# Performance work log

Measured on AMD Instinct MI355X. Metric: run time of the kernel, lower is better.

Reference implementation:

```python
import jax, jax.numpy as jnp
import numpy as np

VOCAB = 128
HID = 1024
STD = 0.01


def setup_inputs() -> dict:
    key = jax.random.key(0)
    ks = jax.random.split(key, 9)
    X = jax.random.randint(ks[0], (64, 512), 0, VOCAB, dtype=jnp.int32)
    def w(k, shape):
        return jax.random.normal(k, shape, dtype=jnp.float32) * STD
    return {
        "X": X,
        # reset gate
        "Wr_x": w(ks[1], (VOCAB, HID)), "Wr_h": w(ks[2], (HID, HID)), "b_r": jnp.zeros(HID, jnp.float32),
        # update gate
        "Wz_x": w(ks[3], (VOCAB, HID)), "Wz_h": w(ks[4], (HID, HID)), "b_z": jnp.zeros(HID, jnp.float32),
        # candidate
        "Wh_x": w(ks[5], (VOCAB, HID)), "Wh_h": w(ks[6], (HID, HID)), "b_h": jnp.zeros(HID, jnp.float32),
        # output head
        "W_o": w(ks[7], (HID, VOCAB)), "b_o": jnp.zeros(VOCAB, jnp.float32),
    }


def reference(X, Wr_x, Wr_h, b_r, Wz_x, Wz_h, b_z, Wh_x, Wh_h, b_h, W_o, b_o):
    B, T = X.shape
    # one-hot encode all timesteps: (T, B, V)
    Xoh = jax.nn.one_hot(X.T, VOCAB, dtype=jnp.float32)

    def step(h, x_t):
        # x_t: (B, V), h: (B, H)
        r = jax.nn.sigmoid(x_t @ Wr_x + h @ Wr_h + b_r)
        z = jax.nn.sigmoid(x_t @ Wz_x + h @ Wz_h + b_z)
        h_tilde = jnp.tanh(x_t @ Wh_x + (r * h) @ Wh_h + b_h)
        h_new = z * h + (1.0 - z) * h_tilde
        out = h_new @ W_o + b_o  # (B, V)
        return h_new, out

    h0 = jnp.zeros((B, HID), jnp.float32)
    _, outs = jax.lax.scan(step, h0, Xoh)  # outs: (T, B, V)
    return jnp.transpose(outs, (1, 0, 2))  # (B, T, V)
```

## Files before the change

### kernel.cpp

```cpp
#include <hip/hip_runtime.h>

#define HID   1024
#define TLEN  512
#define VOC   128
#define NRZ   32
#define NH    32
#define NO    8
#define NBLK  (NRZ + NH + NO)
#define LDSK  1032
#define HBUF  (64 * HID)
#define NHB   8

typedef __bf16 bf16_t;
typedef __attribute__((ext_vector_type(8))) __bf16 bf16x8;
typedef __attribute__((ext_vector_type(4))) float  f32x4;

__device__ __forceinline__ float sigmoid_fast(float x) {
  return 1.0f / (1.0f + __expf(-x));
}
__device__ __forceinline__ float tanh_fast(float x) {
  float e = __expf(-2.0f * x);
  return (1.0f - e) / (1.0f + e);
}

union PairU { bf16_t b[2]; unsigned u; };
union ZPair { float f[2]; unsigned long long u; };


__device__ __forceinline__ void wait_fence(const unsigned* flags, int n, unsigned tgt) {
  if ((threadIdx.x >> 6) == 0) {
    const int lane = threadIdx.x & 63;
    for (;;) {
      unsigned g = tgt;
      if (lane < n)
        g = __hip_atomic_load(&flags[lane], __ATOMIC_RELAXED, __HIP_MEMORY_SCOPE_AGENT);
      if (__all(g >= tgt)) break;
      __builtin_amdgcn_s_sleep(1);
    }
    __builtin_amdgcn_fence(__ATOMIC_ACQUIRE, "agent");
  }
  __syncthreads();
}

__device__ __forceinline__ void wait_nofence(const unsigned* flags, int n, unsigned tgt) {
  if ((threadIdx.x >> 6) == 0) {
    const int lane = threadIdx.x & 63;
    for (;;) {
      unsigned g = tgt;
      if (lane < n)
        g = __hip_atomic_load(&flags[lane], __ATOMIC_RELAXED, __HIP_MEMORY_SCOPE_AGENT);
      if (__all(g >= tgt)) break;
      __builtin_amdgcn_s_sleep(1);
    }
  }
  __syncthreads();
}

__device__ __forceinline__ void wait_rh_out(const unsigned* rfl, const unsigned* ofl,
                                            unsigned tgt, unsigned otgt) {
  if ((threadIdx.x >> 6) == 0) {
    const int lane = threadIdx.x & 63;
    for (;;) {
      bool ok = true;
      if (lane < 32)
        ok = __hip_atomic_load(&rfl[lane], __ATOMIC_RELAXED, __HIP_MEMORY_SCOPE_AGENT) >= tgt;
      else if (lane < 40)
        ok = __hip_atomic_load(&ofl[lane - 32], __ATOMIC_RELAXED, __HIP_MEMORY_SCOPE_AGENT) >= otgt;
      if (__all(ok)) break;
      __builtin_amdgcn_s_sleep(1);
    }
    __builtin_amdgcn_fence(__ATOMIC_ACQUIRE, "agent");
  }
  __syncthreads();
}

__device__ __forceinline__ void publish_rel(unsigned* f, unsigned v) {
  __syncthreads();
  if (threadIdx.x == 0)
    __hip_atomic_store(f, v, __ATOMIC_RELEASE, __HIP_MEMORY_SCOPE_AGENT);
}
__device__ __forceinline__ void publish_rlx(unsigned* f, unsigned v) {
  __syncthreads();
  if (threadIdx.x == 0)
    __hip_atomic_store(f, v, __ATOMIC_RELAXED, __HIP_MEMORY_SCOPE_AGENT);
}

#define MFMA(a, b, c) __builtin_amdgcn_mfma_f32_16x16x32_bf16((a), (b), (c), 0, 0, 0)

__global__ void __launch_bounds__(256)
gru_rz(const int* __restrict__ X,
       const float* __restrict__ Wr_x, const float* __restrict__ Wr_h, const float* __restrict__ b_r,
       const float* __restrict__ Wz_x, const float* __restrict__ Wz_h, const float* __restrict__ b_z,
       const float* __restrict__ Wh_x, const float* __restrict__ Wh_h, const float* __restrict__ b_h,
       const float* __restrict__ W_o,  const float* __restrict__ b_o,
       float* __restrict__ out,
       bf16_t* __restrict__ h0, bf16_t* __restrict__ rh_bf, float* __restrict__ z_f32,
       unsigned* __restrict__ flags)
{
  __shared__ __align__(16) bf16_t Wbuf[2 * 32 * LDSK];

  unsigned* hfl = flags;
  unsigned* rfl = flags + 32;
  unsigned* zfl = flags + 64;
  unsigned* ofl = flags + 96;

  const int blk  = blockIdx.x;
  const int tid  = threadIdx.x;
  const int lane = tid & 63;
  const int wv   = tid >> 6;
  const int n16  = lane & 15;
  const int q    = lane >> 4;

  const int aoff = (wv * 16 + n16) * HID + q * 8;

  int bi[4];
#pragma unroll
  for (int i = 0; i < 4; ++i) bi[i] = wv * 16 + q * 4 + i;

  if (blk < NRZ) {
    const int c0 = blk * 32;
    for (int idx = tid; idx < 32 * HID; idx += 256) {
      int n = idx & 31, k = idx >> 5;
      int r = (n & 1) * 16 + (n >> 1);
      Wbuf[r * LDSK + k]               = (bf16_t)Wr_h[k * HID + c0 + n];
      Wbuf[32 * LDSK + r * LDSK + k]   = (bf16_t)Wz_h[k * HID + c0 + n];
    }
    __syncthreads();

    const int j0 = c0 + 2 * n16;
    const float br0 = b_r[j0], br1 = b_r[j0 + 1];
    const float bz0 = b_z[j0], bz1 = b_z[j0 + 1];
    const bf16_t* wr0 = &Wbuf[n16 * LDSK + q * 8];
    const bf16_t* wr1 = &Wbuf[(16 + n16) * LDSK + q * 8];
    const bf16_t* wz0 = &Wbuf[32 * LDSK + n16 * LDSK + q * 8];
    const bf16_t* wz1 = &Wbuf[32 * LDSK + (16 + n16) * LDSK + q * 8];

    for (int t = 0; t < TLEN; ++t) {
      float gr0[4], gr1[4], gz0[4], gz1[4];
#pragma unroll
      for (int i = 0; i < 4; ++i) {
        int xb = X[bi[i] * TLEN + t];
        gr0[i] = Wr_x[xb * HID + j0];
        gr1[i] = Wr_x[xb * HID + j0 + 1];
        gz0[i] = Wz_x[xb * HID + j0];
        gz1[i] = Wz_x[xb * HID + j0 + 1];
      }
      wait_fence(hfl, NH, (unsigned)t);
      const bf16_t* hslot = h0 + (t & (NHB - 1)) * HBUF;
      const bf16_t* hrow  = hslot + aoff;
      bf16x8 areg[32];
#pragma unroll
      for (int kk = 0; kk < 32; ++kk)
        areg[kk] = *reinterpret_cast<const bf16x8*>(hrow + kk * 32);
      f32x4 a0 = {0.f,0.f,0.f,0.f}, a1 = {0.f,0.f,0.f,0.f};
#pragma unroll
      for (int kk = 0; kk < 32; ++kk) {
        bf16x8 w0 = *reinterpret_cast<const bf16x8*>(wr0 + kk * 32);
        bf16x8 w1 = *reinterpret_cast<const bf16x8*>(wr1 + kk * 32);
        a0 = MFMA(areg[kk], w0, a0);
        a1 = MFMA(areg[kk], w1, a1);
      }
#pragma unroll
      for (int i = 0; i < 4; ++i) {
        int b = bi[i];
        float r0 = sigmoid_fast(a0[i] + br0 + gr0[i]);
        float r1 = sigmoid_fast(a1[i] + br1 + gr1[i]);
        PairU hp = *reinterpret_cast<const PairU*>(hslot + b * HID + j0);
        PairU c;
        c.b[0] = (bf16_t)(r0 * (float)hp.b[0]);
        c.b[1] = (bf16_t)(r1 * (float)hp.b[1]);
        *reinterpret_cast<PairU*>(rh_bf + b * HID + j0) = c;
      }
      publish_rel(&rfl[blk], (unsigned)(t + 1));

      f32x4 c0v = {0.f,0.f,0.f,0.f}, c1v = {0.f,0.f,0.f,0.f};
#pragma unroll
      for (int kk = 0; kk < 32; ++kk) {
        bf16x8 w0 = *reinterpret_cast<const bf16x8*>(wz0 + kk * 32);
        bf16x8 w1 = *reinterpret_cast<const bf16x8*>(wz1 + kk * 32);
        c0v = MFMA(areg[kk], w0, c0v);
        c1v = MFMA(areg[kk], w1, c1v);
      }
#pragma unroll
      for (int i = 0; i < 4; ++i) {
        ZPair zp;
        zp.f[0] = sigmoid_fast(c0v[i] + bz0 + gz0[i]);
        zp.f[1] = sigmoid_fast(c1v[i] + bz1 + gz1[i]);
        __hip_atomic_store((unsigned long long*)(z_f32 + bi[i] * HID + j0), zp.u,
                           __ATOMIC_RELAXED, __HIP_MEMORY_SCOPE_AGENT);
      }
      publish_rlx(&zfl[blk], (unsigned)(t + 1));
    }
  } else if (blk < NRZ + NH) {
    const int hb = blk - NRZ;
    const int c0 = hb * 32;
    for (int idx = tid; idx < 32 * HID; idx += 256) {
      int n = idx & 31, k = idx >> 5;
      int r = (n & 1) * 16 + (n >> 1);
      Wbuf[r * LDSK + k] = (bf16_t)Wh_h[k * HID + c0 + n];
    }
    __syncthreads();

    const int j0 = c0 + 2 * n16;
    const float bh0 = b_h[j0], bh1 = b_h[j0 + 1];
    const bf16_t* wh0 = &Wbuf[n16 * LDSK + q * 8];
    const bf16_t* wh1 = &Wbuf[(16 + n16) * LDSK + q * 8];
    const bf16_t* rhrow = rh_bf + aoff;

    f32x4 hm0 = {0.f,0.f,0.f,0.f}, hm1 = {0.f,0.f,0.f,0.f};

    for (int t = 0; t < TLEN; ++t) {
      float gh0[4], gh1[4];
#pragma unroll
      for (int i = 0; i < 4; ++i) {
        int xb = X[bi[i] * TLEN + t];
        gh0[i] = Wh_x[xb * HID + j0];
        gh1[i] = Wh_x[xb * HID + j0 + 1];
      }
      unsigned otgt = (t + 1 >= NHB) ? (unsigned)(t + 2 - NHB) : 0u;
      wait_rh_out(rfl, ofl, (unsigned)(t + 1), otgt);
      bf16x8 areg[32];
#pragma unroll
      for (int kk = 0; kk < 32; ++kk)
        areg[kk] = *reinterpret_cast<const bf16x8*>(rhrow + kk * 32);
      f32x4 ah0 = {0.f,0.f,0.f,0.f}, ah1 = {0.f,0.f,0.f,0.f};
#pragma unroll
      for (int kk = 0; kk < 32; ++kk) {
        bf16x8 w0 = *reinterpret_cast<const bf16x8*>(wh0 + kk * 32);
        bf16x8 w1 = *reinterpret_cast<const bf16x8*>(wh1 + kk * 32);
        ah0 = MFMA(areg[kk], w0, ah0);
        ah1 = MFMA(areg[kk], w1, ah1);
      }
      wait_nofence(zfl, NRZ, (unsigned)(t + 1));
      bf16_t* hnext = h0 + ((t + 1) & (NHB - 1)) * HBUF;
#pragma unroll
      for (int i = 0; i < 4; ++i) {
        ZPair zp;
        zp.u = __hip_atomic_load((const unsigned long long*)(z_f32 + bi[i] * HID + j0),
                                 __ATOMIC_RELAXED, __HIP_MEMORY_SCOPE_AGENT);
        float ht0 = tanh_fast(ah0[i] + bh0 + gh0[i]);
        float ht1 = tanh_fast(ah1[i] + bh1 + gh1[i]);
        float hn0 = zp.f[0] * hm0[i] + (1.f - zp.f[0]) * ht0;
        float hn1 = zp.f[1] * hm1[i] + (1.f - zp.f[1]) * ht1;
        hm0[i] = hn0; hm1[i] = hn1;
        PairU c; c.b[0] = (bf16_t)hn0; c.b[1] = (bf16_t)hn1;
        *reinterpret_cast<PairU*>(hnext + bi[i] * HID + j0) = c;
      }
      publish_rel(&hfl[hb], (unsigned)(t + 1));
    }
  } else {
    const int ob = blk - NRZ - NH;
    const int c0 = ob * 16;
    for (int idx = tid; idx < 16 * HID; idx += 256) {
      int n = idx & 15, k = idx >> 4;
      Wbuf[n * LDSK + k] = (bf16_t)W_o[k * VOC + c0 + n];
    }
    __syncthreads();

    const int v = c0 + n16;
    const float bos = b_o[v];
    const bf16_t* w0 = &Wbuf[n16 * LDSK + q * 8];

    for (int t = 1; t <= TLEN; ++t) {
      wait_fence(hfl, NH, (unsigned)t);
      const bf16_t* hrow = h0 + (t & (NHB - 1)) * HBUF + aoff;
      bf16x8 areg[32];
#pragma unroll
      for (int kk = 0; kk < 32; ++kk)
        areg[kk] = *reinterpret_cast<const bf16x8*>(hrow + kk * 32);
      f32x4 acc = {0.f,0.f,0.f,0.f};
#pragma unroll
      for (int kk = 0; kk < 32; ++kk) {
        bf16x8 b = *reinterpret_cast<const bf16x8*>(w0 + kk * 32);
        acc = MFMA(areg[kk], b, acc);
      }
#pragma unroll
      for (int i = 0; i < 4; ++i) {
        int b = bi[i];
        out[(b * TLEN + (t - 1)) * VOC + v] = acc[i] + bos;
      }
      publish_rel(&ofl[ob], (unsigned)t);
    }
  }
}

extern "C" void kernel_launch(void* const* d_in, const int* in_sizes, int n_in,
                              void* d_out, int out_size, void* d_ws, size_t ws_size,
                              hipStream_t stream) {
  const int*   X    = (const int*)d_in[0];
  const float* Wr_x = (const float*)d_in[1];
  const float* Wr_h = (const float*)d_in[2];
  const float* b_r  = (const float*)d_in[3];
  const float* Wz_x = (const float*)d_in[4];
  const float* Wz_h = (const float*)d_in[5];
  const float* b_z  = (const float*)d_in[6];
  const float* Wh_x = (const float*)d_in[7];
  const float* Wh_h = (const float*)d_in[8];
  const float* b_h  = (const float*)d_in[9];
  const float* W_o  = (const float*)d_in[10];
  const float* b_o  = (const float*)d_in[11];

  char* ws = (char*)d_ws;
  unsigned* flags = (unsigned*)ws;
  bf16_t*   h0    = (bf16_t*)(ws + 4096);
  bf16_t*   rh_bf = (bf16_t*)(ws + 4096 + NHB * HBUF * sizeof(bf16_t));
  float*    z_f32 = (float*)(ws + 4096 + (NHB + 1) * HBUF * sizeof(bf16_t));

  hipMemsetAsync(ws, 0, 4096 + HBUF * sizeof(bf16_t), stream);

  gru_rz<<<NBLK, 256, 0, stream>>>(
      X, Wr_x, Wr_h, b_r, Wz_x, Wz_h, b_z, Wh_x, Wh_h, b_h, W_o, b_o,
      (float*)d_out, h0, rh_bf, z_f32, flags);
}
```

Measured before the change: 9.184 ms.

## Co-locate recurrent GRU blocks on one XCD and merge r/z/h roles per block

Launches 256 blocks, reads each block's XCC_ID at startup, and elects 32 blocks on a single XCD to run the recurrence; two further blocks compute the output head and the rest exit. Each recurrent block now computes its r, z and candidate slices, keeping z in registers, so the z exchange through global memory and one cross-block wait per step go away. Wr_h and Wh_h stay in LDS while Wz_h is streamed from a global bf16 copy. Acquire/release fences become relaxed flags plus L1 invalidates, relying on the shared L2 within one XCD for coherence, and the output head reads a separate 16-deep h ring. This adds election overhead and depends on the memory-ordering assumptions holding.

```diff
diff --git a/kernel.cpp b/kernel.cpp
--- a/kernel.cpp
+++ b/kernel.cpp
@@ -3,17 +3,18 @@
 #define HID   1024
 #define TLEN  512
 #define VOC   128
-#define NRZ   32
-#define NH    32
-#define NO    8
-#define NBLK  (NRZ + NH + NO)
+#define NBLK  256
+#define NW    32
+#define NO    2
 #define LDSK  1032
 #define HBUF  (64 * HID)
-#define NHB   8
+#define OD    16
 
 typedef __bf16 bf16_t;
 typedef __attribute__((ext_vector_type(8))) __bf16 bf16x8;
 typedef __attribute__((ext_vector_type(4))) float  f32x4;
+typedef __attribute__((ext_vector_type(2))) float  f32x2;
+typedef __attribute__((ext_vector_type(4))) unsigned uint4v;
 
 __device__ __forceinline__ float sigmoid_fast(float x) {
   return 1.0f / (1.0f + __expf(-x));
@@ -24,10 +25,22 @@
 }
 
 union PairU { bf16_t b[2]; unsigned u; };
-union ZPair { float f[2]; unsigned long long u; };
-
-
-__device__ __forceinline__ void wait_fence(const unsigned* flags, int n, unsigned tgt) {
+
+__device__ __forceinline__ void l1_inv() {
+  asm volatile("buffer_inv" ::: "memory");
+}
+
+__device__ __forceinline__ void st_sc1(bf16_t* p, float f0, float f1) {
+  PairU c; c.b[0] = (bf16_t)f0; c.b[1] = (bf16_t)f1;
+  __hip_atomic_store((unsigned*)p, c.u, __ATOMIC_RELAXED, __HIP_MEMORY_SCOPE_AGENT);
+}
+__device__ __forceinline__ bf16x8 ld_nt16(const bf16_t* p) {
+  union { uint4v u; bf16x8 b; } c;
+  c.u = __builtin_nontemporal_load((const uint4v*)p);
+  return c.b;
+}
+
+__device__ __forceinline__ void poll(const unsigned* flags, int n, unsigned tgt) {
   if ((threadIdx.x >> 6) == 0) {
     const int lane = threadIdx.x & 63;
     for (;;) {
@@ -37,49 +50,28 @@
       if (__all(g >= tgt)) break;
       __builtin_amdgcn_s_sleep(1);
     }
-    __builtin_amdgcn_fence(__ATOMIC_ACQUIRE, "agent");
   }
   __syncthreads();
 }
 
-__device__ __forceinline__ void wait_nofence(const unsigned* flags, int n, unsigned tgt) {
-  if ((threadIdx.x >> 6) == 0) {
-    const int lane = threadIdx.x & 63;
-    for (;;) {
-      unsigned g = tgt;
-      if (lane < n)
-        g = __hip_atomic_load(&flags[lane], __ATOMIC_RELAXED, __HIP_MEMORY_SCOPE_AGENT);
-      if (__all(g >= tgt)) break;
-      __builtin_amdgcn_s_sleep(1);
-    }
-  }
-  __syncthreads();
-}
-
-__device__ __forceinline__ void wait_rh_out(const unsigned* rfl, const unsigned* ofl,
-                                            unsigned tgt, unsigned otgt) {
+__device__ __forceinline__ void poll_rf_of(const unsigned* rfl, const unsigned* ofl,
+                                           unsigned tgt, unsigned otgt) {
   if ((threadIdx.x >> 6) == 0) {
     const int lane = threadIdx.x & 63;
     for (;;) {
       bool ok = true;
-      if (lane < 32)
+      if (lane < NW)
         ok = __hip_atomic_load(&rfl[lane], __ATOMIC_RELAXED, __HIP_MEMORY_SCOPE_AGENT) >= tgt;
-      else if (lane < 40)
-        ok = __hip_atomic_load(&ofl[lane - 32], __ATOMIC_RELAXED, __HIP_MEMORY_SCOPE_AGENT) >= otgt;
+      else if (lane < NW + NO)
+        ok = __hip_atomic_load(&ofl[lane - NW], __ATOMIC_RELAXED, __HIP_MEMORY_SCOPE_AGENT) >= otgt;
       if (__all(ok)) break;
       __builtin_amdgcn_s_sleep(1);
     }
-    __builtin_amdgcn_fence(__ATOMIC_ACQUIRE, "agent");
   }
   __syncthreads();
 }
 
-__device__ __forceinline__ void publish_rel(unsigned* f, unsigned v) {
-  __syncthreads();
-  if (threadIdx.x == 0)
-    __hip_atomic_store(f, v, __ATOMIC_RELEASE, __HIP_MEMORY_SCOPE_AGENT);
-}
-__device__ __forceinline__ void publish_rlx(unsigned* f, unsigned v) {
+__device__ __forceinline__ void publish(unsigned* f, unsigned v) {
   __syncthreads();
   if (threadIdx.x == 0)
     __hip_atomic_store(f, v, __ATOMIC_RELAXED, __HIP_MEMORY_SCOPE_AGENT);
@@ -87,199 +79,241 @@
 
 #define MFMA(a, b, c) __builtin_amdgcn_mfma_f32_16x16x32_bf16((a), (b), (c), 0, 0, 0)
 
-__global__ void __launch_bounds__(256)
-gru_rz(const int* __restrict__ X,
-       const float* __restrict__ Wr_x, const float* __restrict__ Wr_h, const float* __restrict__ b_r,
-       const float* __restrict__ Wz_x, const float* __restrict__ Wz_h, const float* __restrict__ b_z,
-       const float* __restrict__ Wh_x, const float* __restrict__ Wh_h, const float* __restrict__ b_h,
-       const float* __restrict__ W_o,  const float* __restrict__ b_o,
-       float* __restrict__ out,
-       bf16_t* __restrict__ h0, bf16_t* __restrict__ rh_bf, float* __restrict__ z_f32,
-       unsigned* __restrict__ flags)
+__global__ void __launch_bounds__(256, 1)
+gru_xcd(const int* __restrict__ X,
+        const float* __restrict__ Wr_x, const float* __restrict__ Wr_h, const float* __restrict__ b_r,
+        const float* __restrict__ Wz_x, const float* __restrict__ Wz_h, const float* __restrict__ b_z,
+        const float* __restrict__ Wh_x, const float* __restrict__ Wh_h, const float* __restrict__ b_h,
+        const float* __restrict__ W_o,  const float* __restrict__ b_o,
+        float* __restrict__ out,
+        bf16_t* __restrict__ hring, bf16_t* __restrict__ rh_bf,
+        bf16_t* __restrict__ oring, bf16_t* __restrict__ wz_bf,
+        unsigned* __restrict__ flags)
 {
   __shared__ __align__(16) bf16_t Wbuf[2 * 32 * LDSK];
-
-  unsigned* hfl = flags;
-  unsigned* rfl = flags + 32;
-  unsigned* zfl = flags + 64;
-  unsigned* ofl = flags + 96;
-
-  const int blk  = blockIdx.x;
+  __shared__ int s_role;
+
+  unsigned* hfl    = flags;
+  unsigned* rfl    = flags + 64;
+  unsigned* ofl    = flags + 128;
+  unsigned* cnt    = flags + 192;
+  unsigned* winner = flags + 200;
+  unsigned* ocnt   = flags + 204;
+
   const int tid  = threadIdx.x;
   const int lane = tid & 63;
   const int wv   = tid >> 6;
   const int n16  = lane & 15;
   const int q    = lane >> 4;
-
   const int aoff = (wv * 16 + n16) * HID + q * 8;
 
   int bi[4];
 #pragma unroll
   for (int i = 0; i < 4; ++i) bi[i] = wv * 16 + q * 4 + i;
 
-  if (blk < NRZ) {
-    const int c0 = blk * 32;
+  if (tid == 0) {
+    unsigned xcc;
+    asm volatile("s_getreg_b32 %0, hwreg(HW_REG_XCC_ID)" : "=s"(xcc));
+    xcc &= 7u;
+    unsigned idx = __hip_atomic_fetch_add(&cnt[xcc], 1u, __ATOMIC_RELAXED, __HIP_MEMORY_SCOPE_AGENT);
+    if (idx == NW - 1) {
+      unsigned exp = 0u;
+      __hip_atomic_compare_exchange_strong(winner, &exp, xcc + 1u,
+          __ATOMIC_RELAXED, __ATOMIC_RELAXED, __HIP_MEMORY_SCOPE_AGENT);
+    }
+    unsigned w;
+    do {
+      w = __hip_atomic_load(winner, __ATOMIC_RELAXED, __HIP_MEMORY_SCOPE_AGENT);
+      __builtin_amdgcn_s_sleep(1);
+    } while (w == 0u);
+    if (xcc == w - 1u && idx < NW) {
+      s_role = (int)idx;
+    } else {
+      unsigned o = __hip_atomic_fetch_add(ocnt, 1u, __ATOMIC_RELAXED, __HIP_MEMORY_SCOPE_AGENT);
+      s_role = (o < NO) ? (NW + (int)o) : -1;
+    }
+  }
+  __syncthreads();
+  const int role = s_role;
+  if (role < 0) return;
+
+  if (role < NW) {
+    const int s  = role;
+    const int c0 = s * 32;
     for (int idx = tid; idx < 32 * HID; idx += 256) {
       int n = idx & 31, k = idx >> 5;
       int r = (n & 1) * 16 + (n >> 1);
-      Wbuf[r * LDSK + k]               = (bf16_t)Wr_h[k * HID + c0 + n];
-      Wbuf[32 * LDSK + r * LDSK + k]   = (bf16_t)Wz_h[k * HID + c0 + n];
-    }
-    __syncthreads();
+      Wbuf[r * LDSK + k]             = (bf16_t)Wr_h[k * HID + c0 + n];
+      Wbuf[32 * LDSK + r * LDSK + k] = (bf16_t)Wh_h[k * HID + c0 + n];
+    }
+    bf16_t* wzs = wz_bf + s * (32 * 1024);
+    for (int idx = tid; idx < 32 * HID; idx += 256) {
+      int n = idx & 31, k = idx >> 5;
+      int r = (n & 1) * 16 + (n >> 1);
+      wzs[r * 1024 + k] = (bf16_t)Wz_h[k * HID + c0 + n];
+    }
 
     const int j0 = c0 + 2 * n16;
+#pragma unroll
+    for (int i = 0; i < 4; ++i) {
+      PairU zz; zz.b[0] = (bf16_t)0.f; zz.b[1] = (bf16_t)0.f;
+      *reinterpret_cast<PairU*>(hring + bi[i] * HID + j0) = zz;
+    }
+    publish(&hfl[s], 1u);
+
     const float br0 = b_r[j0], br1 = b_r[j0 + 1];
     const float bz0 = b_z[j0], bz1 = b_z[j0 + 1];
+    const float bh0 = b_h[j0], bh1 = b_h[j0 + 1];
     const bf16_t* wr0 = &Wbuf[n16 * LDSK + q * 8];
     const bf16_t* wr1 = &Wbuf[(16 + n16) * LDSK + q * 8];
-    const bf16_t* wz0 = &Wbuf[32 * LDSK + n16 * LDSK + q * 8];
-    const bf16_t* wz1 = &Wbuf[32 * LDSK + (16 + n16) * LDSK + q * 8];
+    const bf16_t* wh0 = &Wbuf[32 * LDSK + n16 * LDSK + q * 8];
+    const bf16_t* wh1 = &Wbuf[32 * LDSK + (16 + n16) * LDSK + q * 8];
+    const bf16_t* wz0 = wzs + n16 * 1024 + q * 8;
+    const bf16_t* wz1 = wzs + (16 + n16) * 1024 + q * 8;
+    const bf16_t* rhrow = rh_bf + aoff;
+
+    f32x4 hm0 = {0.f,0.f,0.f,0.f}, hm1 = {0.f,0.f,0.f,0.f};
 
     for (int t = 0; t < TLEN; ++t) {
-      float gr0[4], gr1[4], gz0[4], gz1[4];
+      float gr0[4], gr1[4], gz0[4], gz1[4], gh0[4], gh1[4];
 #pragma unroll
       for (int i = 0; i < 4; ++i) {
         int xb = X[bi[i] * TLEN + t];
-        gr0[i] = Wr_x[xb * HID + j0];
-        gr1[i] = Wr_x[xb * HID + j0 + 1];
-        gz0[i] = Wz_x[xb * HID + j0];
-        gz1[i] = Wz_x[xb * HID + j0 + 1];
-      }
-      wait_fence(hfl, NH, (unsigned)t);
-      const bf16_t* hslot = h0 + (t & (NHB - 1)) * HBUF;
+        gr0[i] = Wr_x[xb * HID + j0]; gr1[i] = Wr_x[xb * HID + j0 + 1];
+        gz0[i] = Wz_x[xb * HID + j0]; gz1[i] = Wz_x[xb * HID + j0 + 1];
+        gh0[i] = Wh_x[xb * HID + j0]; gh1[i] = Wh_x[xb * HID + j0 + 1];
+      }
+      poll(hfl, NW, (unsigned)(t + 1));
+      l1_inv();
+      const bf16_t* hslot = hring + (t & 1) * HBUF;
       const bf16_t* hrow  = hslot + aoff;
       bf16x8 areg[32];
 #pragma unroll
       for (int kk = 0; kk < 32; ++kk)
         areg[kk] = *reinterpret_cast<const bf16x8*>(hrow + kk * 32);
-      f32x4 a0 = {0.f,0.f,0.f,0.f}, a1 = {0.f,0.f,0.f,0.f};
+      f32x4 aR0 = {0.f,0.f,0.f,0.f}, aR1 = {0.f,0.f,0.f,0.f};
 #pragma unroll
       for (int kk = 0; kk < 32; ++kk) {
         bf16x8 w0 = *reinterpret_cast<const bf16x8*>(wr0 + kk * 32);
         bf16x8 w1 = *reinterpret_cast<const bf16x8*>(wr1 + kk * 32);
-        a0 = MFMA(areg[kk], w0, a0);
-        a1 = MFMA(areg[kk], w1, a1);
+        aR0 = MFMA(areg[kk], w0, aR0);
+        aR1 = MFMA(areg[kk], w1, aR1);
       }
 #pragma unroll
       for (int i = 0; i < 4; ++i) {
-        int b = bi[i];
-        float r0 = sigmoid_fast(a0[i] + br0 + gr0[i]);
-        float r1 = sigmoid_fast(a1[i] + br1 + gr1[i]);
-        PairU hp = *reinterpret_cast<const PairU*>(hslot + b * HID + j0);
+        float r0 = sigmoid_fast(aR0[i] + br0 + gr0[i]);
+        float r1 = sigmoid_fast(aR1[i] + br1 + gr1[i]);
+        PairU hp = *reinterpret_cast<const PairU*>(hslot + bi[i] * HID + j0);
         PairU c;
         c.b[0] = (bf16_t)(r0 * (float)hp.b[0]);
         c.b[1] = (bf16_t)(r1 * (float)hp.b[1]);
-        *reinterpret_cast<PairU*>(rh_bf + b * HID + j0) = c;
-      }
-      publish_rel(&rfl[blk], (unsigned)(t + 1));
-
-      f32x4 c0v = {0.f,0.f,0.f,0.f}, c1v = {0.f,0.f,0.f,0.f};
+        *reinterpret_cast<PairU*>(rh_bf + bi[i] * HID + j0) = c;
+      }
+      publish(&rfl[s], (unsigned)(t + 1));
+
+      f32x4 aZ0 = {0.f,0.f,0.f,0.f}, aZ1 = {0.f,0.f,0.f,0.f};
 #pragma unroll
       for (int kk = 0; kk < 32; ++kk) {
         bf16x8 w0 = *reinterpret_cast<const bf16x8*>(wz0 + kk * 32);
         bf16x8 w1 = *reinterpret_cast<const bf16x8*>(wz1 + kk * 32);
-        c0v = MFMA(areg[kk], w0, c0v);
-        c1v = MFMA(areg[kk], w1, c1v);
-      }
+        aZ0 = MFMA(areg[kk], w0, aZ0);
+        aZ1 = MFMA(areg[kk], w1, aZ1);
+      }
+      f32x4 z0, z1;
 #pragma unroll
       for (int i = 0; i < 4; ++i) {
-        ZPair zp;
-        zp.f[0] = sigmoid_fast(c0v[i] + bz0 + gz0[i]);
-        zp.f[1] = sigmoid_fast(c1v[i] + bz1 + gz1[i]);
-        __hip_atomic_store((unsigned long long*)(z_f32 + bi[i] * HID + j0), zp.u,
-                           __ATOMIC_RELAXED, __HIP_MEMORY_SCOPE_AGENT);
-      }
-      publish_rlx(&zfl[blk], (unsigned)(t + 1));
-    }
-  } else if (blk < NRZ + NH) {
-    const int hb = blk - NRZ;
-    const int c0 = hb * 32;
-    for (int idx = tid; idx < 32 * HID; idx += 256) {
-      int n = idx & 31, k = idx >> 5;
-      int r = (n & 1) * 16 + (n >> 1);
-      Wbuf[r * LDSK + k] = (bf16_t)Wh_h[k * HID + c0 + n];
-    }
-    __syncthreads();
-
-    const int j0 = c0 + 2 * n16;
-    const float bh0 = b_h[j0], bh1 = b_h[j0 + 1];
-    const bf16_t* wh0 = &Wbuf[n16 * LDSK + q * 8];
-    const bf16_t* wh1 = &Wbuf[(16 + n16) * LDSK + q * 8];
-    const bf16_t* rhrow = rh_bf + aoff;
-
-    f32x4 hm0 = {0.f,0.f,0.f,0.f}, hm1 = {0.f,0.f,0.f,0.f};
-
-    for (int t = 0; t < TLEN; ++t) {
-      float gh0[4], gh1[4];
-#pragma unroll
-      for (int i = 0; i < 4; ++i) {
-        int xb = X[bi[i] * TLEN + t];
-        gh0[i] = Wh_x[xb * HID + j0];
-        gh1[i] = Wh_x[xb * HID + j0 + 1];
-      }
-      unsigned otgt = (t + 1 >= NHB) ? (unsigned)(t + 2 - NHB) : 0u;
-      wait_rh_out(rfl, ofl, (unsigned)(t + 1), otgt);
-      bf16x8 areg[32];
+        z0[i] = sigmoid_fast(aZ0[i] + bz0 + gz0[i]);
+        z1[i] = sigmoid_fast(aZ1[i] + bz1 + gz1[i]);
+      }
+
+      unsigned otgt = (t > OD - 1) ? (unsigned)(t + 1 - OD) : 0u;
+      poll_rf_of(rfl, ofl, (unsigned)(t + 1), otgt);
+      l1_inv();
+      bf16x8 breg[32];
 #pragma unroll
       for (int kk = 0; kk < 32; ++kk)
-        areg[kk] = *reinterpret_cast<const bf16x8*>(rhrow + kk * 32);
-      f32x4 ah0 = {0.f,0.f,0.f,0.f}, ah1 = {0.f,0.f,0.f,0.f};
+        breg[kk] = *reinterpret_cast<const bf16x8*>(rhrow + kk * 32);
+      f32x4 aH0 = {0.f,0.f,0.f,0.f}, aH1 = {0.f,0.f,0.f,0.f};
 #pragma unroll
       for (int kk = 0; kk < 32; ++kk) {
         bf16x8 w0 = *reinterpret_cast<const bf16x8*>(wh0 + kk * 32);
         bf16x8 w1 = *reinterpret_cast<const bf16x8*>(wh1 + kk * 32);
-        ah0 = MFMA(areg[kk], w0, ah0);
-        ah1 = MFMA(areg[kk], w1, ah1);
-      }
-      wait_nofence(zfl, NRZ, (unsigned)(t + 1));
-      bf16_t* hnext = h0 + ((t + 1) & (NHB - 1)) * HBUF;
+        aH0 = MFMA(breg[kk], w0, aH0);
+        aH1 = MFMA(breg[kk], w1, aH1);
+      }
+      bf16_t* hnext = hring + ((t + 1) & 1) * HBUF;
+      bf16_t* onext = oring + ((t + 1) % OD) * HBUF;
 #pragma unroll
       for (int i = 0; i < 4; ++i) {
-        ZPair zp;
-        zp.u = __hip_atomic_load((const unsigned long long*)(z_f32 + bi[i] * HID + j0),
-                                 __ATOMIC_RELAXED, __HIP_MEMORY_SCOPE_AGENT);
-        float ht0 = tanh_fast(ah0[i] + bh0 + gh0[i]);
-        float ht1 = tanh_fast(ah1[i] + bh1 + gh1[i]);
-        float hn0 = zp.f[0] * hm0[i] + (1.f - zp.f[0]) * ht0;
-        float hn1 = zp.f[1] * hm1[i] + (1.f - zp.f[1]) * ht1;
+        float ht0 = tanh_fast(aH0[i] + bh0 + gh0[i]);
+        float ht1 = tanh_fast(aH1[i] + bh1 + gh1[i]);
+        float hn0 = z0[i] * hm0[i] + (1.f - z0[i]) * ht0;
+        float hn1 = z1[i] * hm1[i] + (1.f - z1[i]) * ht1;
         hm0[i] = hn0; hm1[i] = hn1;
         PairU c; c.b[0] = (bf16_t)hn0; c.b[1] = (bf16_t)hn1;
         *reinterpret_cast<PairU*>(hnext + bi[i] * HID + j0) = c;
-      }
-      publish_rel(&hfl[hb], (unsigned)(t + 1));
-    }
+        st_sc1(onext + bi[i] * HID + j0, hn0, hn1);
+      }
+      publish(&hfl[s], (unsigned)(t + 2));
+    }
+    __builtin_amdgcn_fence(__ATOMIC_RELEASE, "agent");
   } else {
-    const int ob = blk - NRZ - NH;
-    const int c0 = ob * 16;
-    for (int idx = tid; idx < 16 * HID; idx += 256) {
-      int n = idx & 15, k = idx >> 4;
-      Wbuf[n * LDSK + k] = (bf16_t)W_o[k * VOC + c0 + n];
+    const int ob  = role - NW;
+    const int c0o = ob * 64;
+    for (int idx = tid; idx < 64 * HID; idx += 256) {
+      int n = idx & 63, k = idx >> 6;
+      int g = n >> 5, m = n & 31;
+      int r = g * 32 + (m & 1) * 16 + (m >> 1);
+      Wbuf[r * LDSK + k] = (bf16_t)W_o[k * VOC + c0o + n];
     }
     __syncthreads();
 
-    const int v = c0 + n16;
-    const float bos = b_o[v];
-    const bf16_t* w0 = &Wbuf[n16 * LDSK + q * 8];
+    float bo[2][2];
+#pragma unroll
+    for (int g = 0; g < 2; ++g) {
+      bo[g][0] = b_o[c0o + 32 * g + 2 * n16];
+      bo[g][1] = b_o[c0o + 32 * g + 2 * n16 + 1];
+    }
+    const bf16_t* wo[2][2];
+#pragma unroll
+    for (int g = 0; g < 2; ++g)
+#pragma unroll
+      for (int h = 0; h < 2; ++h)
+        wo[g][h] = &Wbuf[(g * 32 + h * 16 + n16) * LDSK + q * 8];
 
     for (int t = 1; t <= TLEN; ++t) {
-      wait_fence(hfl, NH, (unsigned)t);
-      const bf16_t* hrow = h0 + (t & (NHB - 1)) * HBUF + aoff;
+      poll(hfl, NW, (unsigned)(t + 1));
+      const bf16_t* hrow = oring + (t % OD) * HBUF + aoff;
       bf16x8 areg[32];
 #pragma unroll
       for (int kk = 0; kk < 32; ++kk)
-        areg[kk] = *reinterpret_cast<const bf16x8*>(hrow + kk * 32);
-      f32x4 acc = {0.f,0.f,0.f,0.f};
+        areg[kk] = ld_nt16(hrow + kk * 32);
+      f32x4 acc[2][2];
+#pragma unroll
+      for (int g = 0; g < 2; ++g)
+#pragma unroll
+        for (int h = 0; h < 2; ++h)
+          acc[g][h] = (f32x4){0.f, 0.f, 0.f, 0.f};
 #pragma unroll
       for (int kk = 0; kk < 32; ++kk) {
-        bf16x8 b = *reinterpret_cast<const bf16x8*>(w0 + kk * 32);
-        acc = MFMA(areg[kk], b, acc);
-      }
-#pragma unroll
-      for (int i = 0; i < 4; ++i) {
-        int b = bi[i];
-        out[(b * TLEN + (t - 1)) * VOC + v] = acc[i] + bos;
-      }
-      publish_rel(&ofl[ob], (unsigned)t);
+#pragma unroll
+        for (int g = 0; g < 2; ++g) {
+          bf16x8 w0 = *reinterpret_cast<const bf16x8*>(wo[g][0] + kk * 32);
+          bf16x8 w1 = *reinterpret_cast<const bf16x8*>(wo[g][1] + kk * 32);
+          acc[g][0] = MFMA(areg[kk], w0, acc[g][0]);
+          acc[g][1] = MFMA(areg[kk], w1, acc[g][1]);
+        }
+      }
+#pragma unroll
+      for (int g = 0; g < 2; ++g) {
+        const int j0 = c0o + 32 * g + 2 * n16;
+#pragma unroll
+        for (int i = 0; i < 4; ++i) {
+          f32x2 v = {acc[g][0][i] + bo[g][0], acc[g][1][i] + bo[g][1]};
+          *reinterpret_cast<f32x2*>(&out[(bi[i] * TLEN + (t - 1)) * VOC + j0]) = v;
+        }
+      }
+      publish(&ofl[ob], (unsigned)t);
     }
   }
 }
@@ -302,13 +336,14 @@
 
   char* ws = (char*)d_ws;
   unsigned* flags = (unsigned*)ws;
-  bf16_t*   h0    = (bf16_t*)(ws + 4096);
-  bf16_t*   rh_bf = (bf16_t*)(ws + 4096 + NHB * HBUF * sizeof(bf16_t));
-  float*    z_f32 = (float*)(ws + 4096 + (NHB + 1) * HBUF * sizeof(bf16_t));
-
-  hipMemsetAsync(ws, 0, 4096 + HBUF * sizeof(bf16_t), stream);
-
-  gru_rz<<<NBLK, 256, 0, stream>>>(
+  bf16_t*   hring = (bf16_t*)(ws + 4096);
+  bf16_t*   rh_bf = (bf16_t*)(ws + 4096 + 2 * HBUF * sizeof(bf16_t));
+  bf16_t*   oring = (bf16_t*)(ws + 4096 + 3 * HBUF * sizeof(bf16_t));
+  bf16_t*   wz_bf = (bf16_t*)(ws + 4096 + (3 + OD) * HBUF * sizeof(bf16_t));
+
+  hipMemsetAsync(ws, 0, 4096, stream);
+
+  gru_xcd<<<NBLK, 256, 0, stream>>>(
       X, Wr_x, Wr_h, b_r, Wz_x, Wz_h, b_z, Wh_x, Wh_h, b_h, W_o, b_o,
-      (float*)d_out, h0, rh_bf, z_f32, flags);
-}
+      (float*)d_out, hring, rh_bf, oring, wz_bf, flags);
+}
```

Result: faster. 8.456 ms (-7.9%).
